# Optimization experiments

Measured on AMD Instinct MI355X. Metric: run time of the kernel, lower is better.

## Reference

```python
import jax, jax.numpy as jnp
import numpy as np

D = 128          # hidden_dim
H = 4            # num attention heads (torch default nhead=4 in this module)
DH = D // H
NA = 4096        # author nodes
NP = 100000      # paper nodes
EAP = 500000     # author->paper edges
EPA = 500000     # paper->author edges
DFF = 2048       # TransformerEncoderLayer FFN dim (torch default)
OUT = 16
IN_A = 128
IN_P = 256
EPS = 1e-5


def layer_norm(x, g, b):
    mu = jnp.mean(x, -1, keepdims=True)
    var = jnp.mean((x - mu) ** 2, -1, keepdims=True)
    return (x - mu) / jnp.sqrt(var + EPS) * g + b


def scatter_mean(vals, idx, n):
    # torch_scatter 'mean': empty segments yield 0
    s = jax.ops.segment_sum(vals, idx, num_segments=n)
    c = jax.ops.segment_sum(jnp.ones((vals.shape[0], 1), vals.dtype), idx, num_segments=n)
    return s / jnp.maximum(c, 1.0)


def metapath_layer(x_src, x_dst, src, dst, Wv, bv, Wo, bo, g, b):
    # nn.MultiheadAttention applied per-edge with seq_len=1 (query/key/value are
    # [1, E, D]); softmax over a single key is identically 1, so the attention
    # output is exactly out_proj(v_proj(x_src[src])) -- q/k projections have no
    # effect on the output (and zero gradient).
    v = x_src[src] @ Wv.T + bv            # [E, D] gather + value projection
    attn = v @ Wo.T + bo                  # output projection
    agg = scatter_mean(attn, dst, x_dst.shape[0])
    return layer_norm(agg + x_dst, g, b)


def fusion_layer(x, Wqkv, bqkv, Wo, bo, W1, b1, W2, b2, g1, bt1, g2, bt2):
    # torch TransformerEncoderLayer defaults: post-norm, relu, batch_first=False,
    # so x: [S=NA (seq), M (batch = #metapaths), D].
    S, M, _ = x.shape
    qkv = x @ Wqkv.T + bqkv               # [S, M, 3D]
    q, k, v = jnp.split(qkv, 3, axis=-1)
    q = q.reshape(S, M, H, DH)
    k = k.reshape(S, M, H, DH)
    v = v.reshape(S, M, H, DH)
    scores = jnp.einsum('smhd,tmhd->mhst', q, k) / np.float32(np.sqrt(DH))
    a = jax.nn.softmax(scores, axis=-1)
    ctx = jnp.einsum('mhst,tmhd->smhd', a, v).reshape(S, M, D)
    x = layer_norm(x + ctx @ Wo.T + bo, g1, bt1)
    ff = jax.nn.relu(x @ W1.T + b1) @ W2.T + b2
    return layer_norm(x + ff, g2, bt2)


def setup_inputs() -> dict:
    key = jax.random.key(0)
    ks = iter(jax.random.split(key, 64))
    def nrm(shape, scale=0.02):
        return jax.random.normal(next(ks), shape, dtype=jnp.float32) * scale
    inp = {
        'x_author': jax.random.normal(next(ks), (NA, IN_A), dtype=jnp.float32),
        'x_paper': jax.random.normal(next(ks), (NP, IN_P), dtype=jnp.float32),
        'src_ap': jax.random.randint(next(ks), (EAP,), 0, NA),
        'dst_ap': jax.random.randint(next(ks), (EAP,), 0, NP),
        'src_pa': jax.random.randint(next(ks), (EPA,), 0, NP),
        'dst_pa': jax.random.randint(next(ks), (EPA,), 0, NA),
        'pa_W': nrm((D, IN_A)), 'pa_b': nrm((D,)),
        'pp_W': nrm((D, IN_P)), 'pp_b': nrm((D,)),
        'f_Wqkv': nrm((3 * D, D)), 'f_bqkv': nrm((3 * D,)),
        'f_Wo': nrm((D, D)), 'f_bo': nrm((D,)),
        'f_W1': nrm((DFF, D)), 'f_b1': nrm((DFF,)),
        'f_W2': nrm((D, DFF)), 'f_b2': nrm((D,)),
        'f_g1': jnp.ones((D,), jnp.float32), 'f_bt1': jnp.zeros((D,), jnp.float32),
        'f_g2': jnp.ones((D,), jnp.float32), 'f_bt2': jnp.zeros((D,), jnp.float32),
        'cls_W': nrm((OUT, D)), 'cls_b': nrm((OUT,)),
    }
    for i in range(3):
        inp[f'l{i}_Wv'] = nrm((D, D)); inp[f'l{i}_bv'] = nrm((D,))
        inp[f'l{i}_Wo'] = nrm((D, D)); inp[f'l{i}_bo'] = nrm((D,))
        inp[f'l{i}_g'] = jnp.ones((D,), jnp.float32); inp[f'l{i}_b'] = jnp.zeros((D,), jnp.float32)
    return inp


def reference(x_author, x_paper, src_ap, dst_ap, src_pa, dst_pa,
              pa_W, pa_b, pp_W, pp_b,
              f_Wqkv, f_bqkv, f_Wo, f_bo, f_W1, f_b1, f_W2, f_b2,
              f_g1, f_bt1, f_g2, f_bt2, cls_W, cls_b,
              l0_Wv, l0_bv, l0_Wo, l0_bo, l0_g, l0_b,
              l1_Wv, l1_bv, l1_Wo, l1_bo, l1_g, l1_b,
              l2_Wv, l2_bv, l2_Wo, l2_bo, l2_g, l2_b):
    # project node features to hidden_dim
    ha = x_author @ pa_W.T + pa_b         # [NA, D]
    hp = x_paper @ pp_W.T + pp_b          # [NP, D]
    # metapath 0: paper -> author (one MetapathLayer)
    mp0 = metapath_layer(hp, ha, src_pa, dst_pa, l0_Wv, l0_bv, l0_Wo, l0_bo, l0_g, l0_b)
    # metapath 1: author -> paper -> author (two MetapathLayers)
    t = metapath_layer(ha, hp, src_ap, dst_ap, l1_Wv, l1_bv, l1_Wo, l1_bo, l1_g, l1_b)
    mp1 = metapath_layer(t, ha, src_pa, dst_pa, l2_Wv, l2_bv, l2_Wo, l2_bo, l2_g, l2_b)
    stacked = jnp.stack([mp0, mp1], axis=1)   # [NA, 2, D]
    fused = fusion_layer(stacked, f_Wqkv, f_bqkv, f_Wo, f_bo,
                         f_W1, f_b1, f_W2, f_b2,
                         f_g1, f_bt1, f_g2, f_bt2).mean(axis=1)
    return fused @ cls_W.T + cls_b            # [NA, OUT]
```

## Files before the change

kernel.cpp:

```cpp
#include <hip/hip_runtime.h>
#include <math.h>

constexpr int NA = 4096, NP = 100000, E_AP = 500000, E_PA = 500000;
constexpr int D = 128, DFF = 2048, NOUT = 16, IN_A = 128, IN_P = 256;

typedef __attribute__((ext_vector_type(8))) short bf16x8;
typedef __attribute__((ext_vector_type(4))) float f32x4;
typedef unsigned int u32;

__device__ __forceinline__ ushort f2b(float x) {
    union { float f; unsigned u; } v; v.f = x;
    unsigned r = v.u + 0x7fff + ((v.u >> 16) & 1);
    return (ushort)(r >> 16);
}
__device__ __forceinline__ float b2f(ushort h) {
    union { unsigned u; float f; } v; v.u = (unsigned)h << 16;
    return v.f;
}
__device__ __forceinline__ u32 fbits(float x) {
    union { float f; u32 u; } v; v.f = x; return v.u;
}

__device__ __forceinline__ bf16x8 cvtfrag(float4 a, float4 b) {
    union { u32 w[4]; bf16x8 v; } r;
    asm("v_cvt_pk_bf16_f32 %0, %1, %2" : "=v"(r.w[0]) : "v"(a.x), "v"(a.y));
    asm("v_cvt_pk_bf16_f32 %0, %1, %2" : "=v"(r.w[1]) : "v"(a.z), "v"(a.w));
    asm("v_cvt_pk_bf16_f32 %0, %1, %2" : "=v"(r.w[2]) : "v"(b.x), "v"(b.y));
    asm("v_cvt_pk_bf16_f32 %0, %1, %2" : "=v"(r.w[3]) : "v"(b.z), "v"(b.w));
    return r.v;
}

#define GLL(gp, lp) __builtin_amdgcn_global_load_lds( \
    (const __attribute__((address_space(1))) u32*)(gp), \
    (__attribute__((address_space(3))) u32*)(lp), 16, 0, 0)

__global__ __launch_bounds__(256) void gemm_bf16(
    const ushort* __restrict__ Abf, const float* __restrict__ Af32, int lda,
    const ushort* __restrict__ B, int ldb,
    const float* __restrict__ bias,
    float* __restrict__ outf, ushort* __restrict__ outh, int ldc,
    int M, int N, int K, int act)
{
    __shared__ ushort sA[64 * 32];
    __shared__ ushort sB[128 * 32];
    const int wave = threadIdx.x >> 6;
    const int lane = threadIdx.x & 63;
    const int l16 = lane & 15, quad = lane >> 4;
    const int row0 = blockIdx.y * 64;
    const int col0 = blockIdx.x * 128;
    const int wr0 = (wave >> 1) * 32, wc0 = (wave & 1) * 64;
    const int nz = gridDim.z;
    const int ksub = K / nz;
    const int kbeg = blockIdx.z * ksub, kend = kbeg + ksub;

    f32x4 acc[2][4] = {};

    const int sc = lane >> 4, sr = lane & 15;
    const int arow = min(row0 + wave * 16 + sr, M - 1);
    const float*  ap  = Af32 ? Af32 + (long)arow * lda + sc * 8 : nullptr;
    const ushort* abp = Abf  ? Abf  + (long)arow * lda + sc * 8 : nullptr;
    const ushort* bp0 = B + (long)(col0 + (wave * 2) * 16 + sr) * ldb + sc * 8;
    const ushort* bp1 = B + (long)(col0 + (wave * 2 + 1) * 16 + sr) * ldb + sc * 8;

    for (int k0 = kbeg; k0 < kend; k0 += 32) {
        if (k0 != kbeg) __syncthreads();
        if (Af32) {
            float4 f0 = *(const float4*)(ap + k0);
            float4 f1 = *(const float4*)(ap + k0 + 4);
            *(bf16x8*)(sA + wave * 512 + lane * 8) = cvtfrag(f0, f1);
        } else {
            GLL(abp + k0, sA + wave * 512);
        }
        GLL(bp0 + k0, sB + (wave * 2) * 512);
        GLL(bp1 + k0, sB + (wave * 2 + 1) * 512);
        __syncthreads();

        bf16x8 af[2], bfr[4];
        #pragma unroll
        for (int i = 0; i < 2; ++i)
            af[i] = *(const bf16x8*)(sA + ((wr0 >> 4) + i) * 512 + lane * 8);
        #pragma unroll
        for (int j = 0; j < 4; ++j)
            bfr[j] = *(const bf16x8*)(sB + ((wc0 >> 4) + j) * 512 + lane * 8);
        #pragma unroll
        for (int i = 0; i < 2; ++i)
            #pragma unroll
            for (int j = 0; j < 4; ++j)
                acc[i][j] = __builtin_amdgcn_mfma_f32_16x16x32_bf16(
                    af[i], bfr[j], acc[i][j], 0, 0, 0);
    }

    #pragma unroll
    for (int i = 0; i < 2; ++i) {
        #pragma unroll
        for (int r = 0; r < 4; ++r) {
            int row = row0 + wr0 + i * 16 + quad * 4 + r;
            if (row >= M) continue;
            #pragma unroll
            for (int j = 0; j < 4; ++j) {
                int col = col0 + wc0 + j * 16 + l16;
                if (nz > 1) {
                    atomicAdd(&outf[(long)row * ldc + col], acc[i][j][r]);
                } else {
                    float v = acc[i][j][r] + (bias ? bias[col] : 0.f);
                    if (act) v = fmaxf(v, 0.f);
                    if (outf) outf[(long)row * ldc + col] = v;
                    if (outh) outh[(long)row * ldc + col] = f2b(v);
                }
            }
        }
    }
}

__global__ __launch_bounds__(256) void fuse_weights(
    const float* __restrict__ Wv0, const float* __restrict__ bv0,
    const float* __restrict__ Wo0, const float* __restrict__ bo0,
    const float* __restrict__ Wv1, const float* __restrict__ bv1,
    const float* __restrict__ Wo1, const float* __restrict__ bo1,
    const float* __restrict__ Wv2, const float* __restrict__ bv2,
    const float* __restrict__ Wo2, const float* __restrict__ bo2,
    ushort* __restrict__ Wfb, float* __restrict__ beff)
{
    int blk = blockIdx.x;
    if (blk >= 192) {
        int l = blk - 192;
        const float* bv = l == 0 ? bv0 : (l == 1 ? bv1 : bv2);
        const float* Wo = l == 0 ? Wo0 : (l == 1 ? Wo1 : Wo2);
        const float* bo = l == 0 ? bo0 : (l == 1 ? bo1 : bo2);
        if (threadIdx.x < 128) {
            int r = threadIdx.x;
            float acc = bo[r];
            #pragma unroll 8
            for (int j = 0; j < 128; ++j) acc += Wo[r * 128 + j] * bv[j];
            beff[l * 128 + r] = acc;
        }
        return;
    }
    int l = blk >> 6;
    const float* Wv = l == 0 ? Wv0 : (l == 1 ? Wv1 : Wv2);
    const float* Wo = l == 0 ? Wo0 : (l == 1 ? Wo1 : Wo2);
    int r = (blk & 63) * 2 + (threadIdx.x >> 7);
    int c = threadIdx.x & 127;
    float acc = 0.f;
    #pragma unroll 8
    for (int j = 0; j < 128; ++j)
        acc += Wo[r * 128 + j] * Wv[j * 128 + c];
    Wfb[l * 16384 + r * 128 + c] = f2b(acc);
}

__global__ void hist_kernel(const int* __restrict__ dst, int* __restrict__ cnt, int E)
{
    int e = blockIdx.x * 256 + threadIdx.x;
    if (e < E) atomicAdd(&cnt[dst[e]], 1);
}

__global__ __launch_bounds__(256) void scan_local(
    const int* __restrict__ in, int* __restrict__ out,
    int* __restrict__ bsum, int n)
{
    __shared__ int wsum[4];
    int t = threadIdx.x;
    int base = blockIdx.x * 1024 + t * 4;
    int v0 = (base + 0 < n) ? in[base + 0] : 0;
    int v1 = (base + 1 < n) ? in[base + 1] : 0;
    int v2 = (base + 2 < n) ? in[base + 2] : 0;
    int v3 = (base + 3 < n) ? in[base + 3] : 0;
    int tsum = v0 + v1 + v2 + v3;
    int lane = t & 63;
    int x = tsum;
    #pragma unroll
    for (int o = 1; o < 64; o <<= 1) {
        int y = __shfl_up(x, o, 64);
        if (lane >= o) x += y;
    }
    int wid = t >> 6;
    if (lane == 63) wsum[wid] = x;
    __syncthreads();
    int woff = 0;
    #pragma unroll
    for (int ww = 0; ww < 3; ++ww) if (ww < wid) woff += wsum[ww];
    int excl = x - tsum + woff;
    if (base + 0 < n) out[base + 0] = excl;
    if (base + 1 < n) out[base + 1] = excl + v0;
    if (base + 2 < n) out[base + 2] = excl + v0 + v1;
    if (base + 3 < n) out[base + 3] = excl + v0 + v1 + v2;
    if (bsum && t == 255) bsum[blockIdx.x] = excl + tsum;
}

__global__ void scan_add(int* __restrict__ off, const int* __restrict__ bofs, int n)
{
    int i = blockIdx.x * 256 + threadIdx.x;
    if (i < n) off[i] += bofs[i >> 10];
}

__global__ void copy_int_kernel(const int* __restrict__ a, int* __restrict__ b, int n)
{
    int i = blockIdx.x * 256 + threadIdx.x;
    if (i < n) b[i] = a[i];
}

__global__ void fill_csr_kernel(const int* __restrict__ src, const int* __restrict__ dst,
                                int* __restrict__ cur, int* __restrict__ esrc, int E)
{
    int e = blockIdx.x * 256 + threadIdx.x;
    if (e >= E) return;
    int slot = atomicAdd(&cur[dst[e]], 1);
    esrc[slot] = src[e];
}

__global__ __launch_bounds__(256) void gather_mean(
    const ushort* __restrict__ z, const int* __restrict__ off,
    const int* __restrict__ cnt, const int* __restrict__ esrc,
    ushort* __restrict__ outh, int R)
{
    int grp = threadIdx.x >> 5;
    int tg  = threadIdx.x & 31;
    int row = blockIdx.x * 8 + grp;
    if (row >= R) return;
    int e0 = off[row], deg = cnt[row];
    int eend = e0 + deg;
    float a0 = 0.f, a1 = 0.f, a2 = 0.f, a3 = 0.f;
    int e = e0;
    for (; e + 4 <= eend; e += 4) {
        int s0 = esrc[e], s1 = esrc[e + 1], s2 = esrc[e + 2], s3 = esrc[e + 3];
        ushort4 v0 = ((const ushort4*)(z + (long)s0 * 128))[tg];
        ushort4 v1 = ((const ushort4*)(z + (long)s1 * 128))[tg];
        ushort4 v2 = ((const ushort4*)(z + (long)s2 * 128))[tg];
        ushort4 v3 = ((const ushort4*)(z + (long)s3 * 128))[tg];
        a0 += b2f(v0.x) + b2f(v1.x) + b2f(v2.x) + b2f(v3.x);
        a1 += b2f(v0.y) + b2f(v1.y) + b2f(v2.y) + b2f(v3.y);
        a2 += b2f(v0.z) + b2f(v1.z) + b2f(v2.z) + b2f(v3.z);
        a3 += b2f(v0.w) + b2f(v1.w) + b2f(v2.w) + b2f(v3.w);
    }
    for (; e < eend; ++e) {
        int s = esrc[e];
        ushort4 v = ((const ushort4*)(z + (long)s * 128))[tg];
        a0 += b2f(v.x); a1 += b2f(v.y); a2 += b2f(v.z); a3 += b2f(v.w);
    }
    float inv = 1.f / fmaxf((float)deg, 1.f);
    ushort4 h4 = {f2b(a0 * inv), f2b(a1 * inv), f2b(a2 * inv), f2b(a3 * inv)};
    ((ushort4*)(outh + (long)row * 128))[tg] = h4;
}

__global__ __launch_bounds__(256) void gather_mean_ln(
    const ushort* __restrict__ z, const int* __restrict__ off,
    const int* __restrict__ cnt, const int* __restrict__ esrc,
    const ushort* __restrict__ base, const float* __restrict__ g,
    const float* __restrict__ b, ushort* __restrict__ outh, int R)
{
    int grp = threadIdx.x >> 5;
    int tg  = threadIdx.x & 31;
    int row = blockIdx.x * 8 + grp;
    if (row >= R) return;
    int e0 = off[row], deg = cnt[row];
    int eend = e0 + deg;
    float a0 = 0.f, a1 = 0.f, a2 = 0.f, a3 = 0.f;
    int e = e0;
    for (; e + 4 <= eend; e += 4) {
        int s0 = esrc[e], s1 = esrc[e + 1], s2 = esrc[e + 2], s3 = esrc[e + 3];
        ushort4 v0 = ((const ushort4*)(z + (long)s0 * 128))[tg];
        ushort4 v1 = ((const ushort4*)(z + (long)s1 * 128))[tg];
        ushort4 v2 = ((const ushort4*)(z + (long)s2 * 128))[tg];
        ushort4 v3 = ((const ushort4*)(z + (long)s3 * 128))[tg];
        a0 += b2f(v0.x) + b2f(v1.x) + b2f(v2.x) + b2f(v3.x);
        a1 += b2f(v0.y) + b2f(v1.y) + b2f(v2.y) + b2f(v3.y);
        a2 += b2f(v0.z) + b2f(v1.z) + b2f(v2.z) + b2f(v3.z);
        a3 += b2f(v0.w) + b2f(v1.w) + b2f(v2.w) + b2f(v3.w);
    }
    for (; e < eend; ++e) {
        int s = esrc[e];
        ushort4 v = ((const ushort4*)(z + (long)s * 128))[tg];
        a0 += b2f(v.x); a1 += b2f(v.y); a2 += b2f(v.z); a3 += b2f(v.w);
    }
    float inv = 1.f / fmaxf((float)deg, 1.f);
    ushort4 bs = ((const ushort4*)(base + (long)row * 128))[tg];
    float x0 = a0 * inv + b2f(bs.x), x1 = a1 * inv + b2f(bs.y);
    float x2 = a2 * inv + b2f(bs.z), x3 = a3 * inv + b2f(bs.w);
    float s1 = x0 + x1 + x2 + x3;
    #pragma unroll
    for (int o = 1; o < 32; o <<= 1) s1 += __shfl_xor(s1, o, 64);
    float mu = s1 * (1.f / 128.f);
    float d0 = x0 - mu, d1 = x1 - mu, d2 = x2 - mu, d3 = x3 - mu;
    float s2 = d0 * d0 + d1 * d1 + d2 * d2 + d3 * d3;
    #pragma unroll
    for (int o = 1; o < 32; o <<= 1) s2 += __shfl_xor(s2, o, 64);
    float rstd = rsqrtf(s2 * (1.f / 128.f) + 1e-5f);
    float4 gv = ((const float4*)g)[tg];
    float4 bv = ((const float4*)b)[tg];
    ushort4 h4;
    h4.x = f2b(d0 * rstd * gv.x + bv.x);
    h4.y = f2b(d1 * rstd * gv.y + bv.y);
    h4.z = f2b(d2 * rstd * gv.z + bv.z);
    h4.w = f2b(d3 * rstd * gv.w + bv.w);
    ((ushort4*)(outh + (long)row * 128))[tg] = h4;
}

__global__ __launch_bounds__(128) void mean_add_ln(
    const float* __restrict__ a, const float* __restrict__ bias,
    const float* __restrict__ basef, const ushort* __restrict__ baseh,
    const float* __restrict__ g, const float* __restrict__ b,
    float* __restrict__ outf, ushort* __restrict__ outh, int out_ld, int R)
{
    int row = blockIdx.x;
    if (row >= R) return;
    int d = threadIdx.x;
    float x = a[(long)row * 128 + d];
    if (bias) x += bias[d];
    if (basef) x += basef[(long)row * 128 + d];
    if (baseh) x += b2f(baseh[(long)row * 128 + d]);

    __shared__ float red[4];
    float s = x;
    #pragma unroll
    for (int o = 32; o >= 1; o >>= 1) s += __shfl_xor(s, o, 64);
    if ((d & 63) == 0) red[d >> 6] = s;
    __syncthreads();
    float mu = (red[0] + red[1]) * (1.f / 128.f);
    float dx = x - mu;
    float s2 = dx * dx;
    #pragma unroll
    for (int o = 32; o >= 1; o >>= 1) s2 += __shfl_xor(s2, o, 64);
    if ((d & 63) == 0) red[2 + (d >> 6)] = s2;
    __syncthreads();
    float var = (red[2] + red[3]) * (1.f / 128.f);
    float v = dx * rsqrtf(var + 1e-5f) * g[d] + b[d];
    if (outf) outf[(long)row * out_ld + d] = v;
    if (outh) outh[(long)row * out_ld + d] = f2b(v);
}

struct CvtArgs { const float* in[6]; ushort* out[6]; int n4[6]; };
__global__ void cvt_multi(CvtArgs a)
{
    int j = blockIdx.y;
    int i = blockIdx.x * 256 + threadIdx.x;
    if (i >= a.n4[j]) return;
    float4 v = ((const float4*)a.in[j])[i];
    ushort4 o;
    o.x = f2b(v.x); o.y = f2b(v.y); o.z = f2b(v.z); o.w = f2b(v.w);
    ((ushort4*)a.out[j])[i] = o;
}

__global__ __launch_bounds__(256) void flash_attn(
    const ushort* __restrict__ qkvb,
    float* __restrict__ opart, float* __restrict__ lpart_g)
{
    const int qt = blockIdx.x;
    const int mh = blockIdx.y;
    const int ks = blockIdx.z;
    const int m = mh >> 2, h = mh & 3;
    const int wave = threadIdx.x >> 6;
    const int lane = threadIdx.x & 63;
    const int l16 = lane & 15, quad = lane >> 4;

    __shared__ ushort sK[64 * 40];
    __shared__ ushort sV[32 * 72];
    __shared__ ushort sP[4][16 * 72];

    const int q0 = qt * 64 + wave * 16;
    const float qs = 0.17677669529663687f * 1.4426950408889634f;
    bf16x8 qf;
    {
        bf16x8 qraw = *(const bf16x8*)(qkvb + ((long)(q0 + l16) * 2 + m) * 384 + h * 32 + quad * 8);
        #pragma unroll
        for (int j = 0; j < 8; ++j)
            qf[j] = (short)f2b(b2f((ushort)qraw[j]) * qs);
    }

    f32x4 oacc0 = {0.f, 0.f, 0.f, 0.f};
    f32x4 oacc1 = {0.f, 0.f, 0.f, 0.f};
    float lp = 0.f;

    const int kbeg = ks * (NA / 4);
    for (int kt = 0; kt < NA / 4; kt += 64) {
        int k0 = kbeg + kt;
        __syncthreads();
        {
            int key = threadIdx.x >> 2, seg = threadIdx.x & 3;
            bf16x8 kv = *(const bf16x8*)(qkvb + ((long)(k0 + key) * 2 + m) * 384 + 128 + h * 32 + seg * 8);
            *(bf16x8*)(sK + key * 40 + seg * 8) = kv;
        }
        {
            int kp = threadIdx.x & 31, dc = (threadIdx.x >> 5) * 4;
            const ushort* vp = qkvb + ((long)(k0 + kp * 2) * 2 + m) * 384 + 256 + h * 32 + dc;
            ushort4 v0 = *(const ushort4*)vp;
            ushort4 v1 = *(const ushort4*)(vp + 768);
            u32* sv32 = (u32*)sV;
            sv32[(dc + 0) * 36 + kp] = (u32)v0.x | ((u32)v1.x << 16);
            sv32[(dc + 1) * 36 + kp] = (u32)v0.y | ((u32)v1.y << 16);
            sv32[(dc + 2) * 36 + kp] = (u32)v0.z | ((u32)v1.z << 16);
            sv32[(dc + 3) * 36 + kp] = (u32)v0.w | ((u32)v1.w << 16);
        }
        __syncthreads();

        #pragma unroll
        for (int t = 0; t < 4; ++t) {
            bf16x8 kf = *(const bf16x8*)(sK + (t * 16 + l16) * 40 + quad * 8);
            f32x4 s = {0.f, 0.f, 0.f, 0.f};
            s = __builtin_amdgcn_mfma_f32_16x16x32_bf16(kf, qf, s, 0, 0, 0);
            float p0 = exp2f(s[0]), p1 = exp2f(s[1]);
            float p2 = exp2f(s[2]), p3 = exp2f(s[3]);
            lp += (p0 + p1) + (p2 + p3);
            u32 lo = __builtin_amdgcn_perm(fbits(p1), fbits(p0), 0x07060302u);
            u32 hi = __builtin_amdgcn_perm(fbits(p3), fbits(p2), 0x07060302u);
            u32* dst = (u32*)(sP[wave] + l16 * 72 + t * 16 + quad * 4);
            dst[0] = lo; dst[1] = hi;
        }
        #pragma unroll
        for (int c = 0; c < 2; ++c) {
            bf16x8 pf = *(const bf16x8*)(sP[wave] + l16 * 72 + c * 32 + quad * 8);
            bf16x8 v0 = *(const bf16x8*)(sV + l16 * 72 + c * 32 + quad * 8);
            bf16x8 v1 = *(const bf16x8*)(sV + (16 + l16) * 72 + c * 32 + quad * 8);
            oacc0 = __builtin_amdgcn_mfma_f32_16x16x32_bf16(pf, v0, oacc0, 0, 0, 0);
            oacc1 = __builtin_amdgcn_mfma_f32_16x16x32_bf16(pf, v1, oacc1, 0, 0, 0);
        }
    }

    lp += __shfl_xor(lp, 16, 64);
    lp += __shfl_xor(lp, 32, 64);
    if (quad == 0)
        lpart_g[(long)(mh * 4 + ks) * NA + q0 + l16] = lp;

    #pragma unroll
    for (int r = 0; r < 4; ++r) {
        int qr = q0 + quad * 4 + r;
        long ob = ((long)(mh * 4 + ks) * NA + qr) * 32;
        opart[ob + l16]      = oacc0[r];
        opart[ob + 16 + l16] = oacc1[r];
    }
}

__global__ void attn_combine(const float* __restrict__ opart,
                             const float* __restrict__ lpart,
                             ushort* __restrict__ ctxb)
{
    int idx = blockIdx.x * 256 + threadIdx.x;
    int d = idx & 31;
    int row = idx >> 5;
    int mh = row >> 12, qrow = row & 4095;
    float o = 0.f, l = 0.f;
    #pragma unroll
    for (int ks = 0; ks < 4; ++ks) {
        long rb = (long)(mh * 4 + ks) * NA + qrow;
        o += opart[rb * 32 + d];
        l += lpart[rb];
    }
    int m = mh >> 2, h = mh & 3;
    ctxb[((long)qrow * 2 + m) * 128 + h * 32 + d] = f2b(o / l);
}

__global__ void classify_kernel(const float* __restrict__ x2,
                                const float* __restrict__ Wc,
                                const float* __restrict__ bc,
                                float* __restrict__ out)
{
    int idx = blockIdx.x * 256 + threadIdx.x;
    int a2 = idx >> 4, o = idx & 15;
    const float* r0 = x2 + (long)(a2 * 2) * 128;
    const float* r1 = r0 + 128;
    const float* w = Wc + o * 128;
    float acc = bc[o];
    #pragma unroll 4
    for (int dd = 0; dd < 128; ++dd) acc += 0.5f * (r0[dd] + r1[dd]) * w[dd];
    out[idx] = acc;
}

static void bgemm(hipStream_t st, const ushort* Abf, const float* Af32, int lda,
                  const ushort* B, int ldb,
                  const float* bias, float* outf, ushort* outh, int ldc,
                  int M, int N, int K, int act = 0, int ksplit = 1)
{
    dim3 grid(N / 128, (M + 63) / 64, ksplit);
    gemm_bf16<<<grid, 256, 0, st>>>(Abf, Af32, lda, B, ldb, bias, outf, outh,
                                    ldc, M, N, K, act);
}

static void build_csr(hipStream_t st, const int* src, const int* dst, int E, int n,
                      int* cnt, int* off, int* cur, int* bsum, int* esrc)
{
    hipMemsetAsync(cnt, 0, (size_t)n * 4, st);
    hist_kernel<<<(E + 255) / 256, 256, 0, st>>>(dst, cnt, E);
    int nb = (n + 1023) / 1024;
    scan_local<<<nb, 256, 0, st>>>(cnt, off, bsum, n);
    scan_local<<<1, 256, 0, st>>>(bsum, bsum, nullptr, nb);
    scan_add<<<(n + 255) / 256, 256, 0, st>>>(off, bsum, n);
    copy_int_kernel<<<(n + 255) / 256, 256, 0, st>>>(off, cur, n);
    fill_csr_kernel<<<(E + 255) / 256, 256, 0, st>>>(src, dst, cur, esrc, E);
}

extern "C" void kernel_launch(void* const* d_in, const int* in_sizes, int n_in,
                              void* d_out, int out_size, void* d_ws, size_t ws_size,
                              hipStream_t stream)
{
    const float* x_author = (const float*)d_in[0];
    const float* x_paper  = (const float*)d_in[1];
    const int*   src_ap   = (const int*)d_in[2];
    const int*   dst_ap   = (const int*)d_in[3];
    const int*   src_pa   = (const int*)d_in[4];
    const int*   dst_pa   = (const int*)d_in[5];
    const float* pa_W = (const float*)d_in[6];   const float* pa_b = (const float*)d_in[7];
    const float* pp_W = (const float*)d_in[8];   const float* pp_b = (const float*)d_in[9];
    const float* f_Wqkv = (const float*)d_in[10]; const float* f_bqkv = (const float*)d_in[11];
    const float* f_Wo = (const float*)d_in[12];  const float* f_bo = (const float*)d_in[13];
    const float* f_W1 = (const float*)d_in[14];  const float* f_b1 = (const float*)d_in[15];
    const float* f_W2 = (const float*)d_in[16];  const float* f_b2 = (const float*)d_in[17];
    const float* f_g1 = (const float*)d_in[18];  const float* f_bt1 = (const float*)d_in[19];
    const float* f_g2 = (const float*)d_in[20];  const float* f_bt2 = (const float*)d_in[21];
    const float* cls_W = (const float*)d_in[22]; const float* cls_b = (const float*)d_in[23];
    const float* l0_Wv = (const float*)d_in[24]; const float* l0_bv = (const float*)d_in[25];
    const float* l0_Wo = (const float*)d_in[26]; const float* l0_bo = (const float*)d_in[27];
    const float* l0_g  = (const float*)d_in[28]; const float* l0_b  = (const float*)d_in[29];
    const float* l1_Wv = (const float*)d_in[30]; const float* l1_bv = (const float*)d_in[31];
    const float* l1_Wo = (const float*)d_in[32]; const float* l1_bo = (const float*)d_in[33];
    const float* l1_g  = (const float*)d_in[34]; const float* l1_b  = (const float*)d_in[35];
    const float* l2_Wv = (const float*)d_in[36]; const float* l2_bv = (const float*)d_in[37];
    const float* l2_Wo = (const float*)d_in[38]; const float* l2_bo = (const float*)d_in[39];
    const float* l2_g  = (const float*)d_in[40]; const float* l2_b  = (const float*)d_in[41];

    uint8_t* w = (uint8_t*)d_ws;
    ushort* TB  = (ushort*)(w + 0);
    ushort* FF  = (ushort*)(w + 26214400);
    float*  OPART = (float*)(w + 26214400);
    float*  LPART = (float*)(w + 43515904);
    ushort* HPB = (ushort*)(w + 61440000);
    ushort* ZB  = (ushort*)(w + 87040000);
    uint8_t* p2 = w + 102400000;
    ushort* QKVB = (ushort*)(p2 + 0);
    ushort* CTXB = (ushort*)(p2 + 6291456);
    float*  TMP  = (float*)(p2 + 8388608);
    float*  X1   = (float*)(p2 + 12582912);
    ushort* X1B  = (ushort*)(p2 + 16777216);
    float*  TMP2 = (float*)(p2 + 18874368);
    float*  X2   = (float*)(p2 + 23068672);
    uint8_t* tail = p2 + 27262976;
    float*  STKF  = (float*)(tail + 0);
    ushort* STKB  = (ushort*)(tail + 4194304);
    ushort* HAB   = (ushort*)(tail + 6291456);
    ushort* GMA   = (ushort*)(tail + 7340032);
    ushort* WFB   = (ushort*)(tail + 8388608);
    ushort* PAWB  = (ushort*)(tail + 8486912);
    ushort* PPWB  = (ushort*)(tail + 8519680);
    ushort* WQKVB = (ushort*)(tail + 8585216);
    ushort* WOB   = (ushort*)(tail + 8683520);
    ushort* W1B   = (ushort*)(tail + 8716288);
    ushort* W2B   = (ushort*)(tail + 9240576);
    float*  BEFF  = (float*)(tail + 9764864);
    int*   CNT_A  = (int*)(tail + 9766400);
    int*   OFF_A  = (int*)(tail + 9782784);
    int*   CUR_A  = (int*)(tail + 9799168);
    int*   CNT_P  = (int*)(tail + 9815552);
    int*   OFF_P  = (int*)(tail + 10215552);
    int*   CUR_P  = (int*)(tail + 10615552);
    int*   ESRC_PA= (int*)(tail + 11015552);
    int*   ESRC_AP= (int*)(tail + 13015552);
    int*   BSUM_A = (int*)(tail + 15015552);
    int*   BSUM_P = (int*)(tail + 15016576);
    float* TMPA   = (float*)(tail + 15017984);

    CvtArgs ca;
    ca.in[0] = pa_W;   ca.out[0] = PAWB;  ca.n4[0] = D * IN_A / 4;
    ca.in[1] = pp_W;   ca.out[1] = PPWB;  ca.n4[1] = D * IN_P / 4;
    ca.in[2] = f_Wqkv; ca.out[2] = WQKVB; ca.n4[2] = 3 * D * D / 4;
    ca.in[3] = f_Wo;   ca.out[3] = WOB;   ca.n4[3] = D * D / 4;
    ca.in[4] = f_W1;   ca.out[4] = W1B;   ca.n4[4] = DFF * D / 4;
    ca.in[5] = f_W2;   ca.out[5] = W2B;   ca.n4[5] = D * DFF / 4;
    cvt_multi<<<dim3((DFF * D / 4 + 255) / 256, 6), 256, 0, stream>>>(ca);

    fuse_weights<<<195, 256, 0, stream>>>(l0_Wv, l0_bv, l0_Wo, l0_bo,
                                          l1_Wv, l1_bv, l1_Wo, l1_bo,
                                          l2_Wv, l2_bv, l2_Wo, l2_bo, WFB, BEFF);

    build_csr(stream, src_pa, dst_pa, E_PA, NA, CNT_A, OFF_A, CUR_A, BSUM_A, ESRC_PA);
    build_csr(stream, src_ap, dst_ap, E_AP, NP, CNT_P, OFF_P, CUR_P, BSUM_P, ESRC_AP);

    bgemm(stream, nullptr, x_author, IN_A, PAWB, IN_A, pa_b, nullptr, HAB, D, NA, D, IN_A);
    bgemm(stream, nullptr, x_paper,  IN_P, PPWB, IN_P, pp_b, nullptr, HPB, D, NP, D, IN_P);

    gather_mean<<<(NA + 7) / 8, 256, 0, stream>>>(HPB, OFF_A, CNT_A, ESRC_PA, GMA, NA);
    hipMemsetAsync(TMPA, 0, (size_t)NA * D * 4, stream);
    bgemm(stream, GMA, nullptr, D, WFB, D, nullptr, TMPA, nullptr, D, NA, D, D, 0, 4);
    mean_add_ln<<<NA, 128, 0, stream>>>(TMPA, BEFF, nullptr, HAB, l0_g, l0_b,
                                        nullptr, STKB, 256, NA);

    bgemm(stream, HAB, nullptr, D, WFB + 16384, D, BEFF + 128, nullptr, ZB, D, NA, D, D);
    gather_mean_ln<<<(NP + 7) / 8, 256, 0, stream>>>(
        ZB, OFF_P, CNT_P, ESRC_AP, HPB, l1_g, l1_b, TB, NP);

    gather_mean<<<(NA + 7) / 8, 256, 0, stream>>>(TB, OFF_A, CNT_A, ESRC_PA, GMA, NA);
    hipMemsetAsync(TMPA, 0, (size_t)NA * D * 4, stream);
    bgemm(stream, GMA, nullptr, D, WFB + 32768, D, nullptr, TMPA, nullptr, D, NA, D, D, 0, 4);
    mean_add_ln<<<NA, 128, 0, stream>>>(TMPA, BEFF + 256, nullptr, HAB, l2_g, l2_b,
                                        nullptr, STKB + 128, 256, NA);

    bgemm(stream, STKB, nullptr, D, WQKVB, D, f_bqkv, nullptr, QKVB, 3 * D, 2 * NA, 3 * D, D);
    flash_attn<<<dim3(NA / 64, 8, 4), 256, 0, stream>>>(QKVB, OPART, LPART);
    attn_combine<<<8 * NA * 32 / 256, 256, 0, stream>>>(OPART, LPART, CTXB);

    hipMemsetAsync(TMP, 0, (size_t)2 * NA * D * 4, stream);
    bgemm(stream, CTXB, nullptr, D, WOB, D, nullptr, TMP, nullptr, D, 2 * NA, D, D, 0, 4);
    mean_add_ln<<<2 * NA, 128, 0, stream>>>(TMP, f_bo, nullptr, STKB, f_g1, f_bt1,
                                            X1, X1B, 128, 2 * NA);

    bgemm(stream, X1B, nullptr, D, W1B, D, f_b1, nullptr, FF, DFF, 2 * NA, DFF, D, 1);
    hipMemsetAsync(TMP2, 0, (size_t)2 * NA * D * 4, stream);
    bgemm(stream, FF, nullptr, DFF, W2B, DFF, nullptr, TMP2, nullptr, D, 2 * NA, D, DFF, 0, 8);
    mean_add_ln<<<2 * NA, 128, 0, stream>>>(TMP2, f_b2, X1, nullptr, f_g2, f_bt2,
                                            X2, nullptr, 128, 2 * NA);

    classify_kernel<<<(NA * NOUT) / 256, 256, 0, stream>>>(X2, cls_W, cls_b, (float*)d_out);
}
```

Measured before the change: 742.2 us.

## Double-buffer K/V tiles in flash attention with register prefetch and XOR-swizzled LDS

The flash attention kernel now prefetches the next K/V tile into registers while computing on the current one, writes it into a second LDS buffer, and needs only one barrier per iteration instead of two. The padded sV and sP layouts are replaced with XOR-swizzled unpadded layouts to avoid LDS bank conflicts. This is meant to hide global load latency behind MFMA work, at the cost of more LDS and registers, which may lower occupancy.

```diff
diff --git a/kernel.cpp b/kernel.cpp
--- a/kernel.cpp
+++ b/kernel.cpp
@@ -352,9 +352,9 @@
     const int lane = threadIdx.x & 63;
     const int l16 = lane & 15, quad = lane >> 4;
 
-    __shared__ ushort sK[64 * 40];
-    __shared__ ushort sV[32 * 72];
-    __shared__ ushort sP[4][16 * 72];
+    __shared__ ushort sK[2][64 * 40];
+    __shared__ u32    sV[2][32 * 32];
+    __shared__ u32    sP[4][16 * 32];
 
     const int q0 = qt * 64 + wave * 16;
     const float qs = 0.17677669529663687f * 1.4426950408889634f;
@@ -370,31 +370,40 @@
     f32x4 oacc1 = {0.f, 0.f, 0.f, 0.f};
     float lp = 0.f;
 
+    const int skey = threadIdx.x >> 2, sseg = threadIdx.x & 3;
+    const int vkp  = threadIdx.x & 31, vdc  = (threadIdx.x >> 5) * 4;
     const int kbeg = ks * (NA / 4);
-    for (int kt = 0; kt < NA / 4; kt += 64) {
-        int k0 = kbeg + kt;
-        __syncthreads();
-        {
-            int key = threadIdx.x >> 2, seg = threadIdx.x & 3;
-            bf16x8 kv = *(const bf16x8*)(qkvb + ((long)(k0 + key) * 2 + m) * 384 + 128 + h * 32 + seg * 8);
-            *(bf16x8*)(sK + key * 40 + seg * 8) = kv;
+    const ushort* kbase = qkvb + ((long)((kbeg + skey) * 2 + m)) * 384 + 128 + h * 32 + sseg * 8;
+    const ushort* vbase = qkvb + ((long)((kbeg + vkp * 2) * 2 + m)) * 384 + 256 + h * 32 + vdc;
+    const int kwo = skey * 40 + sseg * 8;
+    int vwo[4];
+    #pragma unroll
+    for (int i = 0; i < 4; ++i)
+        vwo[i] = (vdc + i) * 32 + ((((vkp >> 2) ^ ((vdc + i) & 7)) << 2) | (vkp & 3));
+
+    bf16x8 kreg = *(const bf16x8*)(kbase);
+    ushort4 v0r = *(const ushort4*)(vbase);
+    ushort4 v1r = *(const ushort4*)(vbase + 768);
+    *(bf16x8*)(&sK[0][kwo]) = kreg;
+    sV[0][vwo[0]] = (u32)v0r.x | ((u32)v1r.x << 16);
+    sV[0][vwo[1]] = (u32)v0r.y | ((u32)v1r.y << 16);
+    sV[0][vwo[2]] = (u32)v0r.z | ((u32)v1r.z << 16);
+    sV[0][vwo[3]] = (u32)v0r.w | ((u32)v1r.w << 16);
+    __syncthreads();
+
+    int cur = 0;
+    for (int kt = 0; kt < 16; ++kt) {
+        const bool more = (kt + 1) < 16;
+        if (more) {
+            long off = (long)(kt + 1) * 64 * 768;
+            kreg = *(const bf16x8*)(kbase + off);
+            v0r  = *(const ushort4*)(vbase + off);
+            v1r  = *(const ushort4*)(vbase + off + 768);
         }
-        {
-            int kp = threadIdx.x & 31, dc = (threadIdx.x >> 5) * 4;
-            const ushort* vp = qkvb + ((long)(k0 + kp * 2) * 2 + m) * 384 + 256 + h * 32 + dc;
-            ushort4 v0 = *(const ushort4*)vp;
-            ushort4 v1 = *(const ushort4*)(vp + 768);
-            u32* sv32 = (u32*)sV;
-            sv32[(dc + 0) * 36 + kp] = (u32)v0.x | ((u32)v1.x << 16);
-            sv32[(dc + 1) * 36 + kp] = (u32)v0.y | ((u32)v1.y << 16);
-            sv32[(dc + 2) * 36 + kp] = (u32)v0.z | ((u32)v1.z << 16);
-            sv32[(dc + 3) * 36 + kp] = (u32)v0.w | ((u32)v1.w << 16);
-        }
-        __syncthreads();
 
         #pragma unroll
         for (int t = 0; t < 4; ++t) {
-            bf16x8 kf = *(const bf16x8*)(sK + (t * 16 + l16) * 40 + quad * 8);
+            bf16x8 kf = *(const bf16x8*)(&sK[cur][(t * 16 + l16) * 40 + quad * 8]);
             f32x4 s = {0.f, 0.f, 0.f, 0.f};
             s = __builtin_amdgcn_mfma_f32_16x16x32_bf16(kf, qf, s, 0, 0, 0);
             float p0 = exp2f(s[0]), p1 = exp2f(s[1]);
@@ -402,16 +411,29 @@
             lp += (p0 + p1) + (p2 + p3);
             u32 lo = __builtin_amdgcn_perm(fbits(p1), fbits(p0), 0x07060302u);
             u32 hi = __builtin_amdgcn_perm(fbits(p3), fbits(p2), 0x07060302u);
-            u32* dst = (u32*)(sP[wave] + l16 * 72 + t * 16 + quad * 4);
+            u32* dst = &sP[wave][l16 * 32 +
+                                 ((((t * 2 + (quad >> 1)) ^ (l16 & 7)) << 2) | ((quad & 1) * 2))];
             dst[0] = lo; dst[1] = hi;
         }
         #pragma unroll
         for (int c = 0; c < 2; ++c) {
-            bf16x8 pf = *(const bf16x8*)(sP[wave] + l16 * 72 + c * 32 + quad * 8);
-            bf16x8 v0 = *(const bf16x8*)(sV + l16 * 72 + c * 32 + quad * 8);
-            bf16x8 v1 = *(const bf16x8*)(sV + (16 + l16) * 72 + c * 32 + quad * 8);
-            oacc0 = __builtin_amdgcn_mfma_f32_16x16x32_bf16(pf, v0, oacc0, 0, 0, 0);
-            oacc1 = __builtin_amdgcn_mfma_f32_16x16x32_bf16(pf, v1, oacc1, 0, 0, 0);
+            const int gp = ((c * 4 + quad) ^ (l16 & 7)) << 2;
+            bf16x8 pf  = *(const bf16x8*)(&sP[wave][l16 * 32 + gp]);
+            bf16x8 vf0 = *(const bf16x8*)(&sV[cur][l16 * 32 + gp]);
+            bf16x8 vf1 = *(const bf16x8*)(&sV[cur][(16 + l16) * 32 + gp]);
+            oacc0 = __builtin_amdgcn_mfma_f32_16x16x32_bf16(pf, vf0, oacc0, 0, 0, 0);
+            oacc1 = __builtin_amdgcn_mfma_f32_16x16x32_bf16(pf, vf1, oacc1, 0, 0, 0);
+        }
+
+        if (more) {
+            const int nxt = cur ^ 1;
+            *(bf16x8*)(&sK[nxt][kwo]) = kreg;
+            sV[nxt][vwo[0]] = (u32)v0r.x | ((u32)v1r.x << 16);
+            sV[nxt][vwo[1]] = (u32)v0r.y | ((u32)v1r.y << 16);
+            sV[nxt][vwo[2]] = (u32)v0r.z | ((u32)v1r.z << 16);
+            sV[nxt][vwo[3]] = (u32)v0r.w | ((u32)v1r.w << 16);
+            __syncthreads();
+            cur = nxt;
         }
     }
 
```

New measurement: 729.1 us. About the same (-1.8%).
